# Optimization experiments

Measured on AMD Instinct MI355X. Metric: run time of the kernel, lower is better.

## Reference

```python
import jax, jax.numpy as jnp
import numpy as np

DEGREE = 4  # standard ChebyKANLinear default -> 5 basis functions
LN_EPS = 1e-5


def cheby_basis(x, degree=DEGREE):
    # x: [N, D] -> basis [N, D, degree+1] of Chebyshev T_k(tanh(x))
    t = jnp.tanh(x)
    polys = [jnp.ones_like(t), t]
    for _ in range(2, degree + 1):
        polys.append(2.0 * t * polys[-1] - polys[-2])
    return jnp.stack(polys, axis=-1)


def cheby_kan_linear(x, coeffs):
    # coeffs: [in, out, degree+1]
    basis = cheby_basis(x)  # [N, in, degree+1]
    return jnp.einsum('nid,iod->no', basis, coeffs)


def layer_norm(x, gamma, beta):
    mu = jnp.mean(x, axis=-1, keepdims=True)
    var = jnp.mean(jnp.square(x - mu), axis=-1, keepdims=True)
    return (x - mu) * jax.lax.rsqrt(var + LN_EPS) * gamma + beta


def setup_inputs() -> dict:
    key = jax.random.key(0)
    ks = jax.random.split(key, 4)
    N, C, H = 262144, 128, 32
    scale1 = 1.0 / (C * (DEGREE + 1)) ** 0.5
    scale2 = 1.0 / (H * (DEGREE + 1)) ** 0.5
    return {
        'PRV_feat': jax.random.normal(ks[0], (N, C), dtype=jnp.float32),
        'PR_feat': jax.random.normal(ks[1], (N, C), dtype=jnp.float32),
        'coeffs1': jax.random.normal(ks[2], (C, H, DEGREE + 1), dtype=jnp.float32) * scale1,
        'ln_gamma': jnp.ones((H,), dtype=jnp.float32),
        'ln_beta': jnp.zeros((H,), dtype=jnp.float32),
        'coeffs2': jax.random.normal(ks[3], (H, 1, DEGREE + 1), dtype=jnp.float32) * scale2,
        'alpha': jnp.float32(0.5),
    }


def reference(PRV_feat, PR_feat, coeffs1, ln_gamma, ln_beta, coeffs2, alpha):
    # context encoder: ChebyKAN -> LayerNorm -> ReLU
    context = cheby_kan_linear(PR_feat, coeffs1)           # [N, H]
    context = jax.nn.relu(layer_norm(context, ln_gamma, ln_beta))
    # attention gate: ChebyKAN -> Sigmoid, [N, 1]
    attn = jax.nn.sigmoid(cheby_kan_linear(context, coeffs2))
    enhanced = PRV_feat * attn                              # broadcast over channels
    fused = alpha * enhanced + PRV_feat
    return fused
```

## Files before the change

kernel.cpp:

```cpp
#include <hip/hip_runtime.h>
#include <hip/hip_bf16.h>

#define C_DIM 128
#define H_DIM 32

typedef __attribute__((ext_vector_type(8))) short bf16x8;
typedef __attribute__((ext_vector_type(4))) float f32x4;

__device__ __forceinline__ float tanh_fast(float x) {
    float e = __expf(2.0f * x);
    return 1.0f - 2.0f * __builtin_amdgcn_rcpf(e + 1.0f);
}

__device__ __forceinline__ short f2bf(float f) {
    return __builtin_bit_cast(short, __float2bfloat16(f));
}

__global__ void prep_kernel(const float* __restrict__ c1, const float* __restrict__ c2,
                            unsigned short* __restrict__ Bpack, float* __restrict__ bias1,
                            float* __restrict__ E2, float* __restrict__ bias2) {
    const int tid = threadIdx.x;
    const int idx = blockIdx.x * 256 + tid;
    {
        int kc = idx >> 10;
        int oh = (idx >> 9) & 1;
        int l  = (idx >> 3) & 63;
        int j  = idx & 7;
        int g  = l >> 4;
        int kc2 = kc >> 1, kh = kc & 1;
        int c   = kc2 * 16 + 4 * g + 2 * kh + (j >> 2);
        int col = oh * 16 + (l & 15);
        int p   = j & 3;
        const float* cc = c1 + (c * H_DIM + col) * 5;
        float v = (p == 0) ? cc[1] - 3.0f * cc[3]
                : (p == 1) ? 2.0f * cc[2] - 8.0f * cc[4]
                : (p == 2) ? 4.0f * cc[3]
                           : 8.0f * cc[4];
        Bpack[idx] = (unsigned short)f2bf(v);
    }
    if (blockIdx.x == 0) {
        __shared__ float part[256];
        const int o = tid & 31, ch = tid >> 5;
        float b = 0.0f;
        for (int i = ch * 16; i < ch * 16 + 16; ++i) {
            const float* cc = c1 + (i * H_DIM + o) * 5;
            b += cc[0] - cc[2] + cc[4];
        }
        part[tid] = b;
        __syncthreads();
        if (tid < 32) {
            float s = 0.0f;
            #pragma unroll
            for (int k = 0; k < 8; ++k) s += part[k * 32 + tid];
            bias1[tid] = s;
            const float* cc = c2 + tid * 5;
            float4 e;
            e.x = cc[1] - 3.0f * cc[3];
            e.y = 2.0f * cc[2] - 8.0f * cc[4];
            e.z = 4.0f * cc[3];
            e.w = 8.0f * cc[4];
            reinterpret_cast<float4*>(E2)[tid] = e;
        }
        __syncthreads();
        if (tid < 32) part[tid] = c2[tid * 5] - c2[tid * 5 + 2] + c2[tid * 5 + 4];
        __syncthreads();
        if (tid == 0) {
            float b2 = 0.0f;
            for (int h = 0; h < 32; ++h) b2 += part[h];
            bias2[0] = b2;
        }
    }
}

__global__ __launch_bounds__(256, 2) void fused_kernel(
        const float* __restrict__ PRV, const float* __restrict__ PR,
        const unsigned short* __restrict__ Bpack, const float* __restrict__ bias1,
        const float* __restrict__ E2, const float* __restrict__ bias2,
        const float* __restrict__ gamma, const float* __restrict__ beta,
        const float* __restrict__ alphap, float* __restrict__ out) {
    __shared__ char smem[65536];
    float* sPRf = reinterpret_cast<float*>(smem);

    const int tid  = threadIdx.x;
    const int wid  = tid >> 6;
    const int lane = tid & 63;
    const int g    = lane >> 4;
    const int lr   = lane & 15;

    const float4* prsrc = reinterpret_cast<const float4*>(PR) + (size_t)blockIdx.x * 4096;
    #pragma unroll
    for (int i = 0; i < 16; ++i) {
        int fi  = i * 256 + tid;
        int row = fi >> 5;
        int ob  = ((fi & 31) * 16) ^ ((row & 7) << 4);
        *reinterpret_cast<float4*>(smem + row * 512 + ob) = prsrc[fi];
    }
    __syncthreads();

    const float gam0 = gamma[lr], gam1 = gamma[16 + lr];
    const float bet0 = beta[lr],  bet1 = beta[16 + lr];
    const f32x4 e2a = reinterpret_cast<const f32x4*>(E2)[lr];
    const f32x4 e2b = reinterpret_cast<const f32x4*>(E2)[16 + lr];
    const float zb = bias2[0];
    const float alpha = alphap[0];

    f32x4 acc[2][2];
    {
        float b0 = bias1[lr], b1 = bias1[16 + lr];
        #pragma unroll
        for (int t = 0; t < 2; ++t) {
            acc[t][0] = (f32x4){b0, b0, b0, b0};
            acc[t][1] = (f32x4){b1, b1, b1, b1};
        }
    }

    const bf16x8* Bg = reinterpret_cast<const bf16x8*>(Bpack);
    const int rA = wid * 32 + lr;
    const int rB = rA + 16;
    const int swz = (lr & 7) << 4;

    #pragma unroll
    for (int kc2 = 0; kc2 < 8; ++kc2) {
        const int o = kc2 * 64 + g * 16;
        f32x4 x0 = *reinterpret_cast<const f32x4*>(smem + rA * 512 + (o ^ swz));
        f32x4 x1 = *reinterpret_cast<const f32x4*>(smem + rB * 512 + (o ^ swz));
        bf16x8 be0 = Bg[(kc2 * 4 + 0) * 64 + lane];
        bf16x8 be1 = Bg[(kc2 * 4 + 1) * 64 + lane];
        bf16x8 bo0 = Bg[(kc2 * 4 + 2) * 64 + lane];
        bf16x8 bo1 = Bg[(kc2 * 4 + 3) * 64 + lane];
        #define DO_TILE(XC, T) { \
            float t0 = tanh_fast(XC[0]), t1 = tanh_fast(XC[1]); \
            float t2 = tanh_fast(XC[2]), t3 = tanh_fast(XC[3]); \
            float s0 = t0 * t0, s1 = t1 * t1, s2 = t2 * t2, s3 = t3 * t3; \
            bf16x8 ae, ao; \
            ae[0] = f2bf(t0); ae[1] = f2bf(s0); ae[2] = f2bf(s0 * t0); ae[3] = f2bf(s0 * s0); \
            ae[4] = f2bf(t1); ae[5] = f2bf(s1); ae[6] = f2bf(s1 * t1); ae[7] = f2bf(s1 * s1); \
            ao[0] = f2bf(t2); ao[1] = f2bf(s2); ao[2] = f2bf(s2 * t2); ao[3] = f2bf(s2 * s2); \
            ao[4] = f2bf(t3); ao[5] = f2bf(s3); ao[6] = f2bf(s3 * t3); ao[7] = f2bf(s3 * s3); \
            acc[T][0] = __builtin_amdgcn_mfma_f32_16x16x32_bf16(ae, be0, acc[T][0], 0, 0, 0); \
            acc[T][1] = __builtin_amdgcn_mfma_f32_16x16x32_bf16(ae, be1, acc[T][1], 0, 0, 0); \
            acc[T][0] = __builtin_amdgcn_mfma_f32_16x16x32_bf16(ao, bo0, acc[T][0], 0, 0, 0); \
            acc[T][1] = __builtin_amdgcn_mfma_f32_16x16x32_bf16(ao, bo1, acc[T][1], 0, 0, 0); }
        DO_TILE(x0, 0)
        DO_TILE(x1, 1)
        #undef DO_TILE
    }

    #pragma unroll
    for (int t = 0; t < 2; ++t) {
        f32x4 a0 = acc[t][0], a1 = acc[t][1];
        float s[4], vs[4], z[4];
        #pragma unroll
        for (int r = 0; r < 4; ++r) s[r] = a0[r] + a1[r];
        #pragma unroll
        for (int m = 1; m <= 8; m <<= 1) {
            #pragma unroll
            for (int r = 0; r < 4; ++r) s[r] += __shfl_xor(s[r], m, 64);
        }
        #pragma unroll
        for (int r = 0; r < 4; ++r) {
            float mu = s[r] * (1.0f / 32.0f);
            float d0 = a0[r] - mu, d1 = a1[r] - mu;
            a0[r] = d0; a1[r] = d1;
            vs[r] = d0 * d0 + d1 * d1;
        }
        #pragma unroll
        for (int m = 1; m <= 8; m <<= 1) {
            #pragma unroll
            for (int r = 0; r < 4; ++r) vs[r] += __shfl_xor(vs[r], m, 64);
        }
        #pragma unroll
        for (int r = 0; r < 4; ++r) {
            float rs = rsqrtf(vs[r] * (1.0f / 32.0f) + 1e-5f);
            float h0 = fmaf(a0[r] * rs, gam0, bet0);
            float h1 = fmaf(a1[r] * rs, gam1, bet1);
            h0 = fmaxf(h0, 0.0f); h1 = fmaxf(h1, 0.0f);
            float t0 = tanh_fast(h0), t1 = tanh_fast(h1);
            float t02 = t0 * t0, t12 = t1 * t1;
            float zp = fmaf(e2a[0], t0, fmaf(e2a[1], t02,
                        fmaf(e2a[2], t02 * t0, e2a[3] * (t02 * t02))));
            zp += fmaf(e2b[0], t1, fmaf(e2b[1], t12,
                    fmaf(e2b[2], t12 * t1, e2b[3] * (t12 * t12))));
            z[r] = zp;
        }
        #pragma unroll
        for (int m = 1; m <= 8; m <<= 1) {
            #pragma unroll
            for (int r = 0; r < 4; ++r) z[r] += __shfl_xor(z[r], m, 64);
        }
        if (lr == 0) {
            #pragma unroll
            for (int r = 0; r < 4; ++r) {
                float attn = __builtin_amdgcn_rcpf(1.0f + __expf(-(z[r] + zb)));
                sPRf[wid * 4096 + t * 16 + g * 4 + r] = fmaf(alpha, attn, 1.0f);
            }
        }
    }
    __syncthreads();

    const size_t base = (size_t)blockIdx.x * 4096;
    const float4* prv4 = reinterpret_cast<const float4*>(PRV) + base;
    float4* out4 = reinterpret_cast<float4*>(out) + base;
    #pragma unroll 4
    for (int it = 0; it < 16; ++it) {
        int idx = it * 256 + tid;
        int R = idx >> 5;
        float sc = sPRf[(R >> 5) * 4096 + (R & 31)];
        float4 v = prv4[idx];
        v.x *= sc; v.y *= sc; v.z *= sc; v.w *= sc;
        out4[idx] = v;
    }
}

extern "C" void kernel_launch(void* const* d_in, const int* in_sizes, int n_in,
                              void* d_out, int out_size, void* d_ws, size_t ws_size,
                              hipStream_t stream) {
    const float* PRV    = (const float*)d_in[0];
    const float* PR     = (const float*)d_in[1];
    const float* c1     = (const float*)d_in[2];
    const float* gamma  = (const float*)d_in[3];
    const float* beta   = (const float*)d_in[4];
    const float* c2     = (const float*)d_in[5];
    const float* alphap = (const float*)d_in[6];
    float* out = (float*)d_out;

    unsigned short* Bpack = (unsigned short*)d_ws;
    float* wsf   = (float*)((char*)d_ws + 32768);
    float* bias1 = wsf;
    float* E2    = wsf + 32;
    float* bias2 = wsf + 160;

    const int N = in_sizes[0] / C_DIM;

    hipLaunchKernelGGL(prep_kernel, dim3(64), dim3(256), 0, stream,
                       c1, c2, Bpack, bias1, E2, bias2);
    hipLaunchKernelGGL(fused_kernel, dim3(N / 128), dim3(256), 0, stream,
                       PRV, PR, Bpack, bias1, E2, bias2, gamma, beta, alphap, out);
}
```

Measured before the change: 95.59 us.

## Split block into eight independent waves with private LDS slices, dropping block barriers

Each block now runs 512 threads, and each wave owns 16 rows. A wave stages its rows into a private 8KB LDS slice, runs the MFMA, LayerNorm and gate math, then scales its own PRV rows. This removes both block-wide __syncthreads and doubles the waves per block, so memory loads can overlap better with the transcendental and MFMA work. The trade-off is a tighter register budget from launch_bounds(512,4), which could cause spills, and no cross-wave reuse of B fragments per row pair.

Measured after the change: 89.87 us. 6.0% less time.

```diff
diff --git a/kernel.cpp b/kernel.cpp
--- a/kernel.cpp
+++ b/kernel.cpp
@@ -72,30 +72,30 @@
     }
 }
 
-__global__ __launch_bounds__(256, 2) void fused_kernel(
+__global__ __launch_bounds__(512, 4) void fused_kernel(
         const float* __restrict__ PRV, const float* __restrict__ PR,
         const unsigned short* __restrict__ Bpack, const float* __restrict__ bias1,
         const float* __restrict__ E2, const float* __restrict__ bias2,
         const float* __restrict__ gamma, const float* __restrict__ beta,
         const float* __restrict__ alphap, float* __restrict__ out) {
     __shared__ char smem[65536];
-    float* sPRf = reinterpret_cast<float*>(smem);
 
     const int tid  = threadIdx.x;
-    const int wid  = tid >> 6;
+    const int w    = tid >> 6;
     const int lane = tid & 63;
     const int g    = lane >> 4;
     const int lr   = lane & 15;
-
-    const float4* prsrc = reinterpret_cast<const float4*>(PR) + (size_t)blockIdx.x * 4096;
+    char* ws = smem + (w << 13);
+
+    const size_t rowbase = ((size_t)blockIdx.x * 128 + w * 16) * 32;
+    const float4* prsrc = reinterpret_cast<const float4*>(PR) + rowbase;
     #pragma unroll
-    for (int i = 0; i < 16; ++i) {
-        int fi  = i * 256 + tid;
-        int row = fi >> 5;
-        int ob  = ((fi & 31) * 16) ^ ((row & 7) << 4);
-        *reinterpret_cast<float4*>(smem + row * 512 + ob) = prsrc[fi];
-    }
-    __syncthreads();
+    for (int it = 0; it < 8; ++it) {
+        int fi  = it * 64 + lane;
+        int r16 = fi >> 5;
+        int ob  = ((fi & 31) * 16) ^ ((r16 & 7) << 4);
+        *reinterpret_cast<float4*>(ws + r16 * 512 + ob) = prsrc[fi];
+    }
 
     const float gam0 = gamma[lr], gam1 = gamma[16 + lr];
     const float bet0 = beta[lr],  bet1 = beta[16 + lr];
@@ -104,51 +104,41 @@
     const float zb = bias2[0];
     const float alpha = alphap[0];
 
-    f32x4 acc[2][2];
+    f32x4 acc0, acc1;
     {
         float b0 = bias1[lr], b1 = bias1[16 + lr];
-        #pragma unroll
-        for (int t = 0; t < 2; ++t) {
-            acc[t][0] = (f32x4){b0, b0, b0, b0};
-            acc[t][1] = (f32x4){b1, b1, b1, b1};
-        }
+        acc0 = (f32x4){b0, b0, b0, b0};
+        acc1 = (f32x4){b1, b1, b1, b1};
     }
 
     const bf16x8* Bg = reinterpret_cast<const bf16x8*>(Bpack);
-    const int rA = wid * 32 + lr;
-    const int rB = rA + 16;
     const int swz = (lr & 7) << 4;
 
     #pragma unroll
     for (int kc2 = 0; kc2 < 8; ++kc2) {
-        const int o = kc2 * 64 + g * 16;
-        f32x4 x0 = *reinterpret_cast<const f32x4*>(smem + rA * 512 + (o ^ swz));
-        f32x4 x1 = *reinterpret_cast<const f32x4*>(smem + rB * 512 + (o ^ swz));
+        f32x4 x = *reinterpret_cast<const f32x4*>(
+                      ws + lr * 512 + ((kc2 * 64 + g * 16) ^ swz));
         bf16x8 be0 = Bg[(kc2 * 4 + 0) * 64 + lane];
         bf16x8 be1 = Bg[(kc2 * 4 + 1) * 64 + lane];
         bf16x8 bo0 = Bg[(kc2 * 4 + 2) * 64 + lane];
         bf16x8 bo1 = Bg[(kc2 * 4 + 3) * 64 + lane];
-        #define DO_TILE(XC, T) { \
-            float t0 = tanh_fast(XC[0]), t1 = tanh_fast(XC[1]); \
-            float t2 = tanh_fast(XC[2]), t3 = tanh_fast(XC[3]); \
-            float s0 = t0 * t0, s1 = t1 * t1, s2 = t2 * t2, s3 = t3 * t3; \
-            bf16x8 ae, ao; \
-            ae[0] = f2bf(t0); ae[1] = f2bf(s0); ae[2] = f2bf(s0 * t0); ae[3] = f2bf(s0 * s0); \
-            ae[4] = f2bf(t1); ae[5] = f2bf(s1); ae[6] = f2bf(s1 * t1); ae[7] = f2bf(s1 * s1); \
-            ao[0] = f2bf(t2); ao[1] = f2bf(s2); ao[2] = f2bf(s2 * t2); ao[3] = f2bf(s2 * s2); \
-            ao[4] = f2bf(t3); ao[5] = f2bf(s3); ao[6] = f2bf(s3 * t3); ao[7] = f2bf(s3 * s3); \
-            acc[T][0] = __builtin_amdgcn_mfma_f32_16x16x32_bf16(ae, be0, acc[T][0], 0, 0, 0); \
-            acc[T][1] = __builtin_amdgcn_mfma_f32_16x16x32_bf16(ae, be1, acc[T][1], 0, 0, 0); \
-            acc[T][0] = __builtin_amdgcn_mfma_f32_16x16x32_bf16(ao, bo0, acc[T][0], 0, 0, 0); \
-            acc[T][1] = __builtin_amdgcn_mfma_f32_16x16x32_bf16(ao, bo1, acc[T][1], 0, 0, 0); }
-        DO_TILE(x0, 0)
-        DO_TILE(x1, 1)
-        #undef DO_TILE
-    }
-
-    #pragma unroll
-    for (int t = 0; t < 2; ++t) {
-        f32x4 a0 = acc[t][0], a1 = acc[t][1];
+        float t0 = tanh_fast(x[0]), t1 = tanh_fast(x[1]);
+        float t2 = tanh_fast(x[2]), t3 = tanh_fast(x[3]);
+        float s0 = t0 * t0, s1 = t1 * t1, s2 = t2 * t2, s3 = t3 * t3;
+        bf16x8 ae, ao;
+        ae[0] = f2bf(t0); ae[1] = f2bf(s0); ae[2] = f2bf(s0 * t0); ae[3] = f2bf(s0 * s0);
+        ae[4] = f2bf(t1); ae[5] = f2bf(s1); ae[6] = f2bf(s1 * t1); ae[7] = f2bf(s1 * s1);
+        ao[0] = f2bf(t2); ao[1] = f2bf(s2); ao[2] = f2bf(s2 * t2); ao[3] = f2bf(s2 * s2);
+        ao[4] = f2bf(t3); ao[5] = f2bf(s3); ao[6] = f2bf(s3 * t3); ao[7] = f2bf(s3 * s3);
+        acc0 = __builtin_amdgcn_mfma_f32_16x16x32_bf16(ae, be0, acc0, 0, 0, 0);
+        acc1 = __builtin_amdgcn_mfma_f32_16x16x32_bf16(ae, be1, acc1, 0, 0, 0);
+        acc0 = __builtin_amdgcn_mfma_f32_16x16x32_bf16(ao, bo0, acc0, 0, 0, 0);
+        acc1 = __builtin_amdgcn_mfma_f32_16x16x32_bf16(ao, bo1, acc1, 0, 0, 0);
+    }
+
+    float* sw = reinterpret_cast<float*>(ws);
+    {
+        f32x4 a0 = acc0, a1 = acc1;
         float s[4], vs[4], z[4];
         #pragma unroll
         for (int r = 0; r < 4; ++r) s[r] = a0[r] + a1[r];
@@ -192,23 +182,20 @@
             #pragma unroll
             for (int r = 0; r < 4; ++r) {
                 float attn = __builtin_amdgcn_rcpf(1.0f + __expf(-(z[r] + zb)));
-                sPRf[wid * 4096 + t * 16 + g * 4 + r] = fmaf(alpha, attn, 1.0f);
+                sw[g * 4 + r] = fmaf(alpha, attn, 1.0f);
             }
         }
     }
-    __syncthreads();
-
-    const size_t base = (size_t)blockIdx.x * 4096;
-    const float4* prv4 = reinterpret_cast<const float4*>(PRV) + base;
-    float4* out4 = reinterpret_cast<float4*>(out) + base;
-    #pragma unroll 4
-    for (int it = 0; it < 16; ++it) {
-        int idx = it * 256 + tid;
-        int R = idx >> 5;
-        float sc = sPRf[(R >> 5) * 4096 + (R & 31)];
-        float4 v = prv4[idx];
+
+    const float4* prv4 = reinterpret_cast<const float4*>(PRV) + rowbase;
+    float4* out4 = reinterpret_cast<float4*>(out) + rowbase;
+    #pragma unroll
+    for (int it = 0; it < 8; ++it) {
+        int fi = it * 64 + lane;
+        float sc = sw[fi >> 5];
+        float4 v = prv4[fi];
         v.x *= sc; v.y *= sc; v.z *= sc; v.w *= sc;
-        out4[idx] = v;
+        out4[fi] = v;
     }
 }
 
@@ -234,6 +221,6 @@
 
     hipLaunchKernelGGL(prep_kernel, dim3(64), dim3(256), 0, stream,
                        c1, c2, Bpack, bias1, E2, bias2);
-    hipLaunchKernelGGL(fused_kernel, dim3(N / 128), dim3(256), 0, stream,
+    hipLaunchKernelGGL(fused_kernel, dim3(N / 128), dim3(512), 0, stream,
                        PRV, PR, Bpack, bias1, E2, bias2, gamma, beta, alphap, out);
 }
```
